# Kernel tuning notes

Hardware: AMD Instinct MI355X
Metric: run time of the kernel (lower is better)

## Reference

```python
import jax, jax.numpy as jnp
import numpy as np

B, T, C = 4, 2048, 1024
H, DQK, DV = 16, 64, 64
W_SCALE = 0.02  # keep logits in a sane range (mimics GPT-style init)


def setup_inputs() -> dict:
    key = jax.random.key(0)
    k1, k2, k3, k4, k5 = jax.random.split(key, 5)
    x = jax.random.normal(k1, (B, T, C), dtype=jnp.float32)
    Wq = jax.random.normal(k2, (C, H * DQK), dtype=jnp.float32) * W_SCALE
    Wk = jax.random.normal(k3, (C, H * DQK), dtype=jnp.float32) * W_SCALE
    Wv = jax.random.normal(k4, (C, H * DV), dtype=jnp.float32) * W_SCALE
    Wp = jax.random.normal(k5, (DV, C), dtype=jnp.float32) * W_SCALE
    return {"x": x, "Wq": Wq, "Wk": Wk, "Wv": Wv, "Wp": Wp, "iter_num": 0}


def reference(x, Wq, Wk, Wv, Wp, iter_num):
    b, t, c = x.shape
    # projections, split into heads: [B, H, T, D]
    q = (x @ Wq).reshape(b, t, H, DQK).transpose(0, 2, 1, 3)
    k = (x @ Wk).reshape(b, t, H, DQK).transpose(0, 2, 1, 3)
    v = (x @ Wv).reshape(b, t, H, DV).transpose(0, 2, 1, 3)
    scale = 1.0 / jnp.sqrt(jnp.asarray(DQK, dtype=x.dtype))
    att = jnp.einsum('bhqd,bhkd->bhqk', q, k) * scale  # [B,H,T,T]
    causal = jnp.tril(jnp.ones((t, t), dtype=bool))
    att = jnp.where(causal[None, None, :, :], att, -jnp.inf)
    att = jax.nn.softmax(att, axis=-1)
    # att @ v then SUM over heads (not concat): [B, T, DV]
    y = jnp.einsum('bhqk,bhkd->bqd', att, v)
    return y @ Wp  # [B, T, C]
```

## Files before the change

### kernel.cpp

```cpp
#include <hip/hip_runtime.h>
#include <hip/hip_bf16.h>

#define DEVI __device__ __forceinline__

typedef __bf16 bf16x8 __attribute__((ext_vector_type(8)));
typedef float f32x4 __attribute__((ext_vector_type(4)));

DEVI unsigned short f2bf(float x) {
    union { __hip_bfloat16 h; unsigned short u; } v;
    v.h = __float2bfloat16(x);
    return v.u;
}

DEVI float exp2_fast(float x) {
#if __has_builtin(__builtin_amdgcn_exp2f)
    return __builtin_amdgcn_exp2f(x);
#else
    return exp2f(x);
#endif
}

DEVI void gload16(const void* gsrc, void* lds) {
    __builtin_amdgcn_global_load_lds(
        (const __attribute__((address_space(1))) void*)gsrc,
        (__attribute__((address_space(3))) void*)lds,
        16, 0, 0);
}

#define BARRIER_MEM() asm volatile("s_barrier" ::: "memory")
#define WAITVM(n) asm volatile("s_waitcnt vmcnt(" #n ")" ::: "memory")
#define LGKM0() asm volatile("s_waitcnt lgkmcnt(0)" ::: "memory")


__global__ __launch_bounds__(256) void convert_f32_bf16_vec(
    const float* __restrict__ in, unsigned short* __restrict__ out, int n4) {
    int i = blockIdx.x * 256 + threadIdx.x;
    if (i >= n4) return;
    float4 v = reinterpret_cast<const float4*>(in)[i];
    ushort4 o;
    o.x = f2bf(v.x); o.y = f2bf(v.y); o.z = f2bf(v.z); o.w = f2bf(v.w);
    reinterpret_cast<ushort4*>(out)[i] = o;
}

__global__ __launch_bounds__(256) void transpose_wqkv(
    const float* __restrict__ wq, const float* __restrict__ wk,
    const float* __restrict__ wv, unsigned short* __restrict__ dst) {
    __shared__ unsigned short tile[32][33];
    const float* src = (blockIdx.z == 0) ? wq : (blockIdx.z == 1) ? wk : wv;
    unsigned short* d = dst + blockIdx.z * 1024 * 1024;
    int c0 = blockIdx.x * 32, r0 = blockIdx.y * 32;
    int tx = threadIdx.x & 31, ty = threadIdx.x >> 5;
    #pragma unroll
    for (int i = ty; i < 32; i += 8)
        tile[tx][i] = f2bf(src[(r0 + i) * 1024 + c0 + tx]);
    __syncthreads();
    #pragma unroll
    for (int i = ty; i < 32; i += 8)
        d[(c0 + i) * 1024 + r0 + tx] = tile[i][tx];
}

__global__ __launch_bounds__(256) void transpose_f32_to_bf16t(
    const float* __restrict__ src, unsigned short* __restrict__ dst,
    int R, int Cc) {
    __shared__ unsigned short tile[32][33];
    int c0 = blockIdx.x * 32, r0 = blockIdx.y * 32;
    int tx = threadIdx.x & 31, ty = threadIdx.x >> 5;
    #pragma unroll
    for (int i = ty; i < 32; i += 8)
        tile[tx][i] = f2bf(src[(r0 + i) * Cc + c0 + tx]);
    __syncthreads();
    #pragma unroll
    for (int i = ty; i < 32; i += 8)
        dst[(c0 + i) * R + r0 + tx] = tile[i][tx];
}

__global__ __launch_bounds__(256) void transpose_v(
    const unsigned short* __restrict__ vp, unsigned short* __restrict__ vt) {
    __shared__ unsigned short tile[32][33];
    int bh = blockIdx.x;
    int t0 = blockIdx.y * 32;
    int d0 = blockIdx.z * 32;
    int b = bh >> 4, h = bh & 15;
    int tx = threadIdx.x & 31, ty = threadIdx.x >> 5;
    #pragma unroll
    for (int i = ty; i < 32; i += 8)
        tile[tx][i] = vp[(b * 2048 + t0 + i) * 1024 + h * 64 + d0 + tx];
    __syncthreads();
    #pragma unroll
    for (int i = ty; i < 32; i += 8)
        vt[(bh * 64 + d0 + i) * 2048 + t0 + tx] = tile[i][tx];
}

#define LOAD_A8(mh) do { \
    _Pragma("unroll") \
    for (int q = 0; q < 4; ++q) { \
        a[q][0] = *(const bf16x8*)(Arow + ((mh) * 64 + q * 16) * 128 + p16_0); \
        a[q][1] = *(const bf16x8*)(Arow + ((mh) * 64 + q * 16) * 128 + p16_1); \
    } } while (0)

#define LOAD_B4(nh) do { \
    _Pragma("unroll") \
    for (int q2 = 0; q2 < 2; ++q2) { \
        b##nh[q2][0] = *(const bf16x8*)(Brow + ((nh) * 32 + q2 * 16) * 128 + p16_0); \
        b##nh[q2][1] = *(const bf16x8*)(Brow + ((nh) * 32 + q2 * 16) * 128 + p16_1); \
    } } while (0)

#define QUAD(mh, nh) do { \
    __builtin_amdgcn_s_setprio(1); \
    _Pragma("unroll") \
    for (int q = 0; q < 4; ++q) { \
        _Pragma("unroll") \
        for (int q2 = 0; q2 < 2; ++q2) { \
            acc[(mh) * 4 + q][(nh) * 2 + q2] = __builtin_amdgcn_mfma_f32_16x16x32_bf16( \
                a[q][0], b##nh[q2][0], acc[(mh) * 4 + q][(nh) * 2 + q2], 0, 0, 0); \
            acc[(mh) * 4 + q][(nh) * 2 + q2] = __builtin_amdgcn_mfma_f32_16x16x32_bf16( \
                a[q][1], b##nh[q2][1], acc[(mh) * 4 + q][(nh) * 2 + q2], 0, 0, 0); \
        } } \
    __builtin_amdgcn_s_setprio(0); } while (0)

__global__ __launch_bounds__(512, 2) void gemm256(
    const unsigned short* __restrict__ A, const unsigned short* __restrict__ Bt,
    unsigned short* __restrict__ q_out, unsigned short* __restrict__ k_out,
    unsigned short* __restrict__ v_out) {
    __shared__ unsigned short Ab[2][256 * 64];
    __shared__ unsigned short Bb[2][256 * 64];

    const int wg = (blockIdx.x & 7) * 48 + (blockIdx.x >> 3);
    const int bm = (wg / 12) << 8;
    const int bn = (wg % 12) << 8;

    const int tid = threadIdx.x;
    const int w = tid >> 6, l = tid & 63;
    const int wm = w >> 2, wn = w & 3;
    const int lc = l & 15, lg = l >> 4;
    const int lr8 = l >> 3;
    const int colsw = 8 * ((l & 7) ^ lr8);

    const unsigned short* gA = A + (size_t)(bm + lr8) * 1024 + colsw;
    const unsigned short* gB = Bt + (size_t)(bn + lr8) * 1024 + colsw;

    const int p16_0 = ((lg) ^ (lc & 7)) * 16;
    const int p16_1 = ((4 | lg) ^ (lc & 7)) * 16;

    auto STAGE_A = [&](int h, int bufn, int tt) {
        #pragma unroll
        for (int j = 0; j < 2; ++j) {
            const int row0 = wm * 128 + h * 64 + ((((w & 3) << 1) | j) << 3);
            gload16(gA + row0 * 1024 + tt * 64, (char*)&Ab[bufn][0] + row0 * 128);
        }
    };
    auto STAGE_B = [&](int g, int bufn, int tt) {
        #pragma unroll
        for (int j = 0; j < 2; ++j) {
            const int row0 = (w >> 1) * 64 + g * 32 + ((((w & 1) << 1) | j) << 3);
            gload16(gB + row0 * 1024 + tt * 64, (char*)&Bb[bufn][0] + row0 * 128);
        }
    };

    bf16x8 a[4][2], b0[2][2], b1[2][2];
    f32x4 acc[8][4] = {};

    const int nt = 16;

    STAGE_A(0, 0, 0); STAGE_B(0, 0, 0); STAGE_B(1, 0, 0); STAGE_A(1, 0, 0);
    STAGE_A(0, 1, 1); STAGE_B(0, 1, 1); STAGE_B(1, 1, 1);

    #pragma unroll 1
    for (int t = 0; t < nt; ++t) {
        const int buf = t & 1;
        const char* Arow = (const char*)&Ab[buf][0] + (wm * 128 + lc) * 128;
        const char* Brow = (const char*)&Bb[buf][0] + (wn * 64 + lc) * 128;
        if (t == nt - 1) { WAITVM(0); } else { WAITVM(6); }
        BARRIER_MEM();
        LOAD_A8(0);
        LOAD_B4(0);
        if (t + 1 < nt) STAGE_A(1, buf ^ 1, t + 1);
        BARRIER_MEM(); LGKM0();
        QUAD(0, 0);
        BARRIER_MEM();
        LOAD_B4(1);
        if (t + 2 < nt) STAGE_A(0, buf, t + 2);
        BARRIER_MEM(); LGKM0();
        QUAD(0, 1);
        BARRIER_MEM();
        LOAD_A8(1);
        if (t + 2 < nt) STAGE_B(0, buf, t + 2);
        BARRIER_MEM(); LGKM0();
        QUAD(1, 1);
        BARRIER_MEM();
        if (t + 2 < nt) STAGE_B(1, buf, t + 2);
        BARRIER_MEM();
        QUAD(1, 0);
    }

    const int whichsel = bn >> 10;
    unsigned short* dst = (whichsel == 0) ? q_out : (whichsel == 1) ? k_out : v_out;
    const int rrbase = (bn & 1023) + wn * 64 + lc;
    #pragma unroll
    for (int mi = 0; mi < 8; ++mi) {
        #pragma unroll
        for (int r = 0; r < 4; ++r) {
            const int m = bm + wm * 128 + mi * 16 + lg * 4 + r;
            #pragma unroll
            for (int ni = 0; ni < 4; ++ni)
                dst[(size_t)m * 1024 + rrbase + ni * 16] = f2bf(acc[mi][ni][r]);
        }
    }
}

template <int EPI>
__global__ __launch_bounds__(256) void gemm_bt(
    const unsigned short* __restrict__ A, const unsigned short* __restrict__ Bt,
    int Mdim, int Ndim, int Kdim,
    unsigned short* __restrict__ q_out, unsigned short* __restrict__ k_out,
    unsigned short* __restrict__ v_out, float* __restrict__ c_out) {
    __shared__ unsigned short As[128 * 32];
    __shared__ unsigned short Bs[128 * 32];
    const int ntn = Ndim >> 7;
    const int bm = (blockIdx.x / ntn) << 7;
    const int bn = (blockIdx.x % ntn) << 7;
    const int tid = threadIdx.x;
    const int w = tid >> 6, l = tid & 63;
    const int wr = w >> 1, wc = w & 1;
    const int lrow = l >> 2, lcb = (l & 3) * 8;
    const int lc = l & 15, lg = l >> 4;

    f32x4 acc[4][4] = {};

    for (int k0 = 0; k0 < Kdim; k0 += 32) {
        __syncthreads();
        #pragma unroll
        for (int i = 0; i < 2; ++i) {
            int j = w * 2 + i;
            gload16(A + (bm + j * 16 + lrow) * Kdim + k0 + lcb, (char*)As + j * 1024);
            gload16(Bt + (bn + j * 16 + lrow) * Kdim + k0 + lcb, (char*)Bs + j * 1024);
        }
        __syncthreads();
        bf16x8 af[4], bfr[4];
        #pragma unroll
        for (int mi = 0; mi < 4; ++mi)
            af[mi] = *reinterpret_cast<const bf16x8*>(&As[(wr * 64 + mi * 16 + lc) * 32 + lg * 8]);
        #pragma unroll
        for (int ni = 0; ni < 4; ++ni)
            bfr[ni] = *reinterpret_cast<const bf16x8*>(&Bs[(wc * 64 + ni * 16 + lc) * 32 + lg * 8]);
        #pragma unroll
        for (int mi = 0; mi < 4; ++mi)
            #pragma unroll
            for (int ni = 0; ni < 4; ++ni)
                acc[mi][ni] = __builtin_amdgcn_mfma_f32_16x16x32_bf16(
                    af[mi], bfr[ni], acc[mi][ni], 0, 0, 0);
    }

    #pragma unroll
    for (int mi = 0; mi < 4; ++mi) {
        #pragma unroll
        for (int ni = 0; ni < 4; ++ni) {
            #pragma unroll
            for (int r = 0; r < 4; ++r) {
                int m = bm + wr * 64 + mi * 16 + lg * 4 + r;
                int n = bn + wc * 64 + ni * 16 + lc;
                float val = acc[mi][ni][r];
                if (EPI == 0) {
                    int which = n >> 10, rr = n & 1023;
                    unsigned short* dst = (which == 0) ? q_out : (which == 1) ? k_out : v_out;
                    dst[m * 1024 + rr] = f2bf(val);
                } else {
                    c_out[m * Ndim + n] = val;
                }
            }
        }
    }
}

__global__ __launch_bounds__(512, 4) void attn_kernel(
    const unsigned short* __restrict__ qb, const unsigned short* __restrict__ kb,
    const unsigned short* __restrict__ vt, unsigned short* __restrict__ ypart) {
    __shared__ unsigned short Ks[2][64 * 64];
    __shared__ unsigned short Vs[2][64 * 64];
    __shared__ unsigned short plds[8][16 * 72];

    const int i = blockIdx.x;
    const int slot = i >> 3;
    const int bh = (i & 7) + ((slot >> 3) << 3);
    const int pr = slot & 7;
    const int b = bh >> 4, h = bh & 15;
    const int tid = threadIdx.x, w = tid >> 6, l = tid & 63;
    const int lc = l & 15, lg = l >> 4;

    const float SCL = 0.125f * 1.44269504f;

    const int rowc = l >> 3;
    const int colsw = 8 * ((l & 7) ^ rowc);
    const unsigned short* kbh = kb + (b * 2048) * 1024 + h * 64;
    const unsigned short* vbh = vt + bh * 64 * 2048;
    const int swz = (lc & 7) * 8;

    unsigned short* pl = &plds[w][0];

    auto STAGE = [&](int bufn, int kt) {
        const int tk0s = kt << 6;
        const int row = w * 8 + rowc;
        gload16(kbh + (tk0s + row) * 1024 + colsw, (char*)&Ks[bufn][0] + w * 1024);
        gload16(vbh + row * 2048 + tk0s + colsw, (char*)&Vs[bufn][0] + w * 1024);
    };

    auto run_pass = [&](int qblk) {
        const int q0 = qblk << 7;
        const int qrowW = q0 + w * 16;

        bf16x8 qf[2];
        {
            const unsigned short* qp =
                qb + (b * 2048 + qrowW + lc) * 1024 + h * 64;
            qf[0] = *reinterpret_cast<const bf16x8*>(qp + lg * 8);
            qf[1] = *reinterpret_cast<const bf16x8*>(qp + 32 + lg * 8);
        }

        f32x4 accO[4] = {};
        float lsum[4] = {};

        const int nkt = 2 * qblk + 2;
        STAGE(0, 0);

        for (int kt = 0; kt < nkt; ++kt) {
            const int cur = kt & 1;
            const int tk0 = kt << 6;
            if (kt + 1 < nkt) {
                STAGE(cur ^ 1, kt + 1);
                WAITVM(2);
            } else {
                WAITVM(0);
            }
            BARRIER_MEM();

            if (tk0 <= qrowW + 15) {
                f32x4 s[4] = {};
                #pragma unroll
                for (int ni = 0; ni < 4; ++ni) {
                    const unsigned short* kr = &Ks[cur][(ni * 16 + lc) * 64];
                    bf16x8 kf0 = *reinterpret_cast<const bf16x8*>(&kr[(lg * 8) ^ swz]);
                    bf16x8 kf1 = *reinterpret_cast<const bf16x8*>(&kr[(32 + lg * 8) ^ swz]);
                    s[ni] = __builtin_amdgcn_mfma_f32_16x16x32_bf16(qf[0], kf0, s[ni], 0, 0, 0);
                    s[ni] = __builtin_amdgcn_mfma_f32_16x16x32_bf16(qf[1], kf1, s[ni], 0, 0, 0);
                }
                const bool needmask = (tk0 + 63 > qrowW);
                #pragma unroll
                for (int ni = 0; ni < 4; ++ni) {
                    #pragma unroll
                    for (int r = 0; r < 4; ++r) {
                        float sv = s[ni][r] * SCL;
                        if (needmask) {
                            int tq = qrowW + lg * 4 + r;
                            int tk = tk0 + ni * 16 + lc;
                            sv = (tk > tq) ? -INFINITY : sv;
                        }
                        float pv = exp2_fast(sv);
                        lsum[r] += pv;
                        pl[(lg * 4 + r) * 72 + ni * 16 + lc] = f2bf(pv);
                    }
                }
                bf16x8 pf0 = *reinterpret_cast<const bf16x8*>(&pl[lc * 72 + lg * 8]);
                bf16x8 pf1 = *reinterpret_cast<const bf16x8*>(&pl[lc * 72 + 32 + lg * 8]);
                #pragma unroll
                for (int ni = 0; ni < 4; ++ni) {
                    const unsigned short* vr = &Vs[cur][(ni * 16 + lc) * 64];
                    bf16x8 vf0 = *reinterpret_cast<const bf16x8*>(&vr[(lg * 8) ^ swz]);
                    bf16x8 vf1 = *reinterpret_cast<const bf16x8*>(&vr[(32 + lg * 8) ^ swz]);
                    accO[ni] = __builtin_amdgcn_mfma_f32_16x16x32_bf16(pf0, vf0, accO[ni], 0, 0, 0);
                    accO[ni] = __builtin_amdgcn_mfma_f32_16x16x32_bf16(pf1, vf1, accO[ni], 0, 0, 0);
                }
            }
            BARRIER_MEM();
        }

        #pragma unroll
        for (int r = 0; r < 4; ++r) {
            float t = lsum[r];
            #pragma unroll
            for (int msk = 1; msk <= 8; msk <<= 1)
                t += __shfl_xor(t, msk);
            float rinv = 1.0f / t;
            int tq = qrowW + lg * 4 + r;
            #pragma unroll
            for (int ni = 0; ni < 4; ++ni)
                ypart[(bh * 2048 + tq) * 64 + ni * 16 + lc] =
                    f2bf(accO[ni][r] * rinv);
        }
    };

    run_pass(15 - pr);
    run_pass(pr);
}

__global__ __launch_bounds__(256) void reduce_heads(
    const unsigned short* __restrict__ ypart, unsigned short* __restrict__ yb) {
    int idx = blockIdx.x * 256 + threadIdx.x;
    int d = idx & 63, m = idx >> 6;
    int b = m >> 11, t = m & 2047;
    const unsigned short* p = ypart + ((b * 16) * 2048 + t) * 64 + d;
    float s = 0.f;
    #pragma unroll
    for (int h = 0; h < 16; ++h) {
        union { unsigned short u; __hip_bfloat16 h; } v;
        v.u = p[h * 2048 * 64];
        s += __bfloat162float(v.h);
    }
    yb[idx] = f2bf(s);
}


extern "C" void kernel_launch(void* const* d_in, const int* in_sizes, int n_in,
                              void* d_out, int out_size, void* d_ws, size_t ws_size,
                              hipStream_t stream) {
    const float* x  = (const float*)d_in[0];
    const float* Wq = (const float*)d_in[1];
    const float* Wk = (const float*)d_in[2];
    const float* Wv = (const float*)d_in[3];
    const float* Wp = (const float*)d_in[4];
    float* out = (float*)d_out;

    if (ws_size < 91357184) return;
    char* ws = (char*)d_ws;
    unsigned short* ypart = (unsigned short*)ws;
    unsigned short* xb   = (unsigned short*)ws;
    unsigned short* vprj = (unsigned short*)(ws + 16777216);
    unsigned short* wt   = (unsigned short*)(ws + 33554432);
    unsigned short* wpt  = (unsigned short*)(ws + 39845888);
    unsigned short* qbf  = (unsigned short*)(ws + 39976960);
    unsigned short* kbf  = (unsigned short*)(ws + 56754176);
    unsigned short* vtb  = (unsigned short*)(ws + 73531392);
    unsigned short* yb   = (unsigned short*)(ws + 90308608);

    convert_f32_bf16_vec<<<8192, 256, 0, stream>>>(x, xb, 2097152);
    transpose_wqkv<<<dim3(32, 32, 3), 256, 0, stream>>>(Wq, Wk, Wv, wt);
    transpose_f32_to_bf16t<<<dim3(32, 2), 256, 0, stream>>>(Wp, wpt, 64, 1024);

    gemm256<<<384, 512, 0, stream>>>(xb, wt, qbf, kbf, vprj);

    transpose_v<<<dim3(64, 64, 2), 256, 0, stream>>>(vprj, vtb);

    attn_kernel<<<512, 512, 0, stream>>>(qbf, kbf, vtb, ypart);

    reduce_heads<<<2048, 256, 0, stream>>>(ypart, yb);

    gemm_bt<1><<<(8192 / 128) * (1024 / 128), 256, 0, stream>>>(
        yb, wpt, 8192, 1024, 64, nullptr, nullptr, nullptr, out);
}
```

Measured before the change: 169.3 us.

## Fuse V transpose into QKV GEMM epilogue and triple-buffer attention K/V tiles

The QKV projection GEMM now writes the V slice directly in transposed [bh, d, t] layout with 4-wide packed stores, which removes the separate transpose_v kernel and its extra round trip through global memory. The attention kernel grows from double to triple buffering of K/V tiles in LDS, so loads run two tiles ahead and the end-of-iteration barrier is dropped. It also swaps the MFMA operand order so each lane holds a whole query row, which allows packed bf16 conversion of P, a single scalar row sum with fewer shuffles, and vectorized output stores. The cost is more LDS per block, which may reduce occupancy, and V stores from the GEMM that are strided rather than contiguous.

```diff
diff --git a/kernel.cpp b/kernel.cpp
--- a/kernel.cpp
+++ b/kernel.cpp
@@ -72,23 +72,6 @@
     #pragma unroll
     for (int i = ty; i < 32; i += 8)
         dst[(c0 + i) * R + r0 + tx] = tile[i][tx];
-}
-
-__global__ __launch_bounds__(256) void transpose_v(
-    const unsigned short* __restrict__ vp, unsigned short* __restrict__ vt) {
-    __shared__ unsigned short tile[32][33];
-    int bh = blockIdx.x;
-    int t0 = blockIdx.y * 32;
-    int d0 = blockIdx.z * 32;
-    int b = bh >> 4, h = bh & 15;
-    int tx = threadIdx.x & 31, ty = threadIdx.x >> 5;
-    #pragma unroll
-    for (int i = ty; i < 32; i += 8)
-        tile[tx][i] = vp[(b * 2048 + t0 + i) * 1024 + h * 64 + d0 + tx];
-    __syncthreads();
-    #pragma unroll
-    for (int i = ty; i < 32; i += 8)
-        vt[(bh * 64 + d0 + i) * 2048 + t0 + tx] = tile[i][tx];
 }
 
 #define LOAD_A8(mh) do { \
@@ -194,16 +177,34 @@
     }
 
     const int whichsel = bn >> 10;
-    unsigned short* dst = (whichsel == 0) ? q_out : (whichsel == 1) ? k_out : v_out;
     const int rrbase = (bn & 1023) + wn * 64 + lc;
-    #pragma unroll
-    for (int mi = 0; mi < 8; ++mi) {
-        #pragma unroll
-        for (int r = 0; r < 4; ++r) {
-            const int m = bm + wm * 128 + mi * 16 + lg * 4 + r;
+    if (whichsel == 2) {
+        #pragma unroll
+        for (int mi = 0; mi < 8; ++mi) {
+            const int m = bm + wm * 128 + mi * 16 + lg * 4;
+            const int bb = m >> 11, tt = m & 2047;
             #pragma unroll
-            for (int ni = 0; ni < 4; ++ni)
-                dst[(size_t)m * 1024 + rrbase + ni * 16] = f2bf(acc[mi][ni][r]);
+            for (int ni = 0; ni < 4; ++ni) {
+                const int rr = rrbase + ni * 16;
+                const int bhh = bb * 16 + (rr >> 6), d = rr & 63;
+                ushort4 o;
+                o.x = f2bf(acc[mi][ni][0]); o.y = f2bf(acc[mi][ni][1]);
+                o.z = f2bf(acc[mi][ni][2]); o.w = f2bf(acc[mi][ni][3]);
+                *reinterpret_cast<ushort4*>(
+                    &v_out[((size_t)bhh * 64 + d) * 2048 + tt]) = o;
+            }
+        }
+    } else {
+        unsigned short* dst = (whichsel == 0) ? q_out : k_out;
+        #pragma unroll
+        for (int mi = 0; mi < 8; ++mi) {
+            #pragma unroll
+            for (int r = 0; r < 4; ++r) {
+                const int m = bm + wm * 128 + mi * 16 + lg * 4 + r;
+                #pragma unroll
+                for (int ni = 0; ni < 4; ++ni)
+                    dst[(size_t)m * 1024 + rrbase + ni * 16] = f2bf(acc[mi][ni][r]);
+            }
         }
     }
 }
@@ -275,8 +276,8 @@
 __global__ __launch_bounds__(512, 4) void attn_kernel(
     const unsigned short* __restrict__ qb, const unsigned short* __restrict__ kb,
     const unsigned short* __restrict__ vt, unsigned short* __restrict__ ypart) {
-    __shared__ unsigned short Ks[2][64 * 64];
-    __shared__ unsigned short Vs[2][64 * 64];
+    __shared__ unsigned short Ks[3][64 * 64];
+    __shared__ unsigned short Vs[3][64 * 64];
     __shared__ unsigned short plds[8][16 * 72];
 
     const int i = blockIdx.x;
@@ -317,21 +318,21 @@
         }
 
         f32x4 accO[4] = {};
-        float lsum[4] = {};
+        float lsum = 0.f;
 
         const int nkt = 2 * qblk + 2;
         STAGE(0, 0);
+        STAGE(1, 1);
+        int cur = 0;
 
         for (int kt = 0; kt < nkt; ++kt) {
-            const int cur = kt & 1;
             const int tk0 = kt << 6;
-            if (kt + 1 < nkt) {
-                STAGE(cur ^ 1, kt + 1);
-                WAITVM(2);
-            } else {
-                WAITVM(0);
+            if (kt + 1 < nkt) { WAITVM(2); } else { WAITVM(0); }
+            BARRIER_MEM();
+            if (kt + 2 < nkt) {
+                const int sb = (cur >= 1) ? cur - 1 : cur + 2;
+                STAGE(sb, kt + 2);
             }
-            BARRIER_MEM();
 
             if (tk0 <= qrowW + 15) {
                 f32x4 s[4] = {};
@@ -340,24 +341,29 @@
                     const unsigned short* kr = &Ks[cur][(ni * 16 + lc) * 64];
                     bf16x8 kf0 = *reinterpret_cast<const bf16x8*>(&kr[(lg * 8) ^ swz]);
                     bf16x8 kf1 = *reinterpret_cast<const bf16x8*>(&kr[(32 + lg * 8) ^ swz]);
-                    s[ni] = __builtin_amdgcn_mfma_f32_16x16x32_bf16(qf[0], kf0, s[ni], 0, 0, 0);
-                    s[ni] = __builtin_amdgcn_mfma_f32_16x16x32_bf16(qf[1], kf1, s[ni], 0, 0, 0);
+                    s[ni] = __builtin_amdgcn_mfma_f32_16x16x32_bf16(kf0, qf[0], s[ni], 0, 0, 0);
+                    s[ni] = __builtin_amdgcn_mfma_f32_16x16x32_bf16(kf1, qf[1], s[ni], 0, 0, 0);
                 }
                 const bool needmask = (tk0 + 63 > qrowW);
+                const int tq = qrowW + lc;
                 #pragma unroll
                 for (int ni = 0; ni < 4; ++ni) {
+                    float pv[4];
                     #pragma unroll
                     for (int r = 0; r < 4; ++r) {
                         float sv = s[ni][r] * SCL;
                         if (needmask) {
-                            int tq = qrowW + lg * 4 + r;
-                            int tk = tk0 + ni * 16 + lc;
+                            int tk = tk0 + ni * 16 + lg * 4 + r;
                             sv = (tk > tq) ? -INFINITY : sv;
                         }
-                        float pv = exp2_fast(sv);
-                        lsum[r] += pv;
-                        pl[(lg * 4 + r) * 72 + ni * 16 + lc] = f2bf(pv);
+                        pv[r] = exp2_fast(sv);
+                        lsum += pv[r];
                     }
+                    unsigned int w0, w1;
+                    asm("v_cvt_pk_bf16_f32 %0, %1, %2" : "=v"(w0) : "v"(pv[0]), "v"(pv[1]));
+                    asm("v_cvt_pk_bf16_f32 %0, %1, %2" : "=v"(w1) : "v"(pv[2]), "v"(pv[3]));
+                    uint2 pk2; pk2.x = w0; pk2.y = w1;
+                    *reinterpret_cast<uint2*>(&pl[lc * 72 + ni * 16 + lg * 4]) = pk2;
                 }
                 bf16x8 pf0 = *reinterpret_cast<const bf16x8*>(&pl[lc * 72 + lg * 8]);
                 bf16x8 pf1 = *reinterpret_cast<const bf16x8*>(&pl[lc * 72 + 32 + lg * 8]);
@@ -366,25 +372,28 @@
                     const unsigned short* vr = &Vs[cur][(ni * 16 + lc) * 64];
                     bf16x8 vf0 = *reinterpret_cast<const bf16x8*>(&vr[(lg * 8) ^ swz]);
                     bf16x8 vf1 = *reinterpret_cast<const bf16x8*>(&vr[(32 + lg * 8) ^ swz]);
-                    accO[ni] = __builtin_amdgcn_mfma_f32_16x16x32_bf16(pf0, vf0, accO[ni], 0, 0, 0);
-                    accO[ni] = __builtin_amdgcn_mfma_f32_16x16x32_bf16(pf1, vf1, accO[ni], 0, 0, 0);
+                    accO[ni] = __builtin_amdgcn_mfma_f32_16x16x32_bf16(vf0, pf0, accO[ni], 0, 0, 0);
+                    accO[ni] = __builtin_amdgcn_mfma_f32_16x16x32_bf16(vf1, pf1, accO[ni], 0, 0, 0);
                 }
             }
-            BARRIER_MEM();
-        }
-
-        #pragma unroll
-        for (int r = 0; r < 4; ++r) {
-            float t = lsum[r];
-            #pragma unroll
-            for (int msk = 1; msk <= 8; msk <<= 1)
-                t += __shfl_xor(t, msk);
-            float rinv = 1.0f / t;
-            int tq = qrowW + lg * 4 + r;
-            #pragma unroll
-            for (int ni = 0; ni < 4; ++ni)
-                ypart[(bh * 2048 + tq) * 64 + ni * 16 + lc] =
-                    f2bf(accO[ni][r] * rinv);
+            cur = (cur + 1 == 3) ? 0 : cur + 1;
+        }
+        BARRIER_MEM();
+
+        float tsum = lsum;
+        tsum += __shfl_xor(tsum, 16);
+        tsum += __shfl_xor(tsum, 32);
+        const float rinv = 1.0f / tsum;
+        const int tq = qrowW + lc;
+        #pragma unroll
+        for (int ni = 0; ni < 4; ++ni) {
+            ushort4 o;
+            o.x = f2bf(accO[ni][0] * rinv);
+            o.y = f2bf(accO[ni][1] * rinv);
+            o.z = f2bf(accO[ni][2] * rinv);
+            o.w = f2bf(accO[ni][3] * rinv);
+            *reinterpret_cast<ushort4*>(
+                &ypart[(bh * 2048 + tq) * 64 + ni * 16 + lg * 4]) = o;
         }
     };
 
@@ -423,7 +432,6 @@
     char* ws = (char*)d_ws;
     unsigned short* ypart = (unsigned short*)ws;
     unsigned short* xb   = (unsigned short*)ws;
-    unsigned short* vprj = (unsigned short*)(ws + 16777216);
     unsigned short* wt   = (unsigned short*)(ws + 33554432);
     unsigned short* wpt  = (unsigned short*)(ws + 39845888);
     unsigned short* qbf  = (unsigned short*)(ws + 39976960);
@@ -435,9 +443,7 @@
     transpose_wqkv<<<dim3(32, 32, 3), 256, 0, stream>>>(Wq, Wk, Wv, wt);
     transpose_f32_to_bf16t<<<dim3(32, 2), 256, 0, stream>>>(Wp, wpt, 64, 1024);
 
-    gemm256<<<384, 512, 0, stream>>>(xb, wt, qbf, kbf, vprj);
-
-    transpose_v<<<dim3(64, 64, 2), 256, 0, stream>>>(vprj, vtb);
+    gemm256<<<384, 512, 0, stream>>>(xb, wt, qbf, kbf, vtb);
 
     attn_kernel<<<512, 512, 0, stream>>>(qbf, kbf, vtb, ypart);
 
```

Result: faster. 161.4 us (-4.7%).
